# Performance work log

Measured on AMD Instinct MI355X. Metric: run time of the kernel, lower is better.

Reference implementation:

```python
import jax, jax.numpy as jnp
import numpy as np

S, H, I, E, TOP_K = 8192, 2048, 2048, 8, 2


def setup_inputs() -> dict:
    key = jax.random.key(0)
    k0, k1, k2, k3 = jax.random.split(key, 4)
    scale = 1.0 / np.sqrt(H)
    return {
        "hidden_states": jax.random.normal(k0, (S, H), dtype=jnp.float32),
        "w_gate": jax.random.normal(k1, (E, H), dtype=jnp.float32) * scale,
        "w1": jax.random.normal(k2, (E, 2 * I, H), dtype=jnp.float32) * scale,
        "w2": jax.random.normal(k3, (E, H, I), dtype=jnp.float32) * (1.0 / np.sqrt(I)),
        "top_k": TOP_K,
    }


def reference(hidden_states, w_gate, w1, w2, top_k):
    # Router: logits -> float32 softmax -> top-k -> renormalize
    router_logits = hidden_states @ w_gate.T                      # [S, E]
    probs = jax.nn.softmax(router_logits.astype(jnp.float32), axis=-1)
    top_p, top_i = jax.lax.top_k(probs, top_k)                    # [S, k]
    top_p = top_p / jnp.sum(top_p, axis=-1, keepdims=True)

    n_tok, n_exp = probs.shape
    # Dense combine weights [S, E]; zero for non-selected experts.
    combine = jnp.zeros((n_tok, n_exp), dtype=probs.dtype)
    combine = combine.at[jnp.arange(n_tok)[:, None], top_i].add(top_p)

    inter = w2.shape[2]
    out = jnp.zeros_like(hidden_states)
    # Loop over the small fixed expert set; masked-combine gives exact
    # fused_moe semantics (scatter-combine of weighted expert outputs).
    for e in range(n_exp):
        gu = hidden_states @ w1[e].T                              # [S, 2I]
        gate, up = gu[:, :inter], gu[:, inter:]
        h = jax.nn.silu(gate) * up                                # SiluAndMul
        out = out + combine[:, e:e + 1].astype(hidden_states.dtype) * (h @ w2[e].T)
    return out, router_logits
```

## Files before the change

### kernel.cpp

```cpp
#include <hip/hip_runtime.h>
#include <hip/hip_bf16.h>
#include <stdint.h>

#define S_TOK 8192
#define H_DIM 2048
#define I_DIM 2048
#define E_NUM 8

typedef __attribute__((ext_vector_type(4))) float f32x4;
typedef __attribute__((ext_vector_type(8))) short bf16x8;

#define MFMA16(a, b, c) __builtin_amdgcn_mfma_f32_16x16x32_bf16((a), (b), (c), 0, 0, 0)

__device__ __forceinline__ unsigned short f2bf(float f) {
    unsigned int u = __float_as_uint(f);
    unsigned int r = (u + 0x7FFFu + ((u >> 16) & 1u)) >> 16;
    return (unsigned short)r;
}
__device__ __forceinline__ float bf2f(unsigned short u) {
    return __uint_as_float((unsigned int)u << 16);
}

__device__ __forceinline__ void async_copy16(void* lds, const void* g) {
    __builtin_amdgcn_global_load_lds(
        (const __attribute__((address_space(1))) void*)(uintptr_t)g,
        (__attribute__((address_space(3))) void*)(uintptr_t)lds,
        16, 0, 0);
}

__device__ __forceinline__ int xcd_swizzle(int bid, int nwg) {
    int cpx = nwg >> 3;
    return (bid & 7) * cpx + (bid >> 3);
}

__global__ void cvt_kernel(const float* __restrict__ src, unsigned short* __restrict__ dst, long n) {
    long i0 = ((long)blockIdx.x * blockDim.x + threadIdx.x) * 4;
    long stride = (long)gridDim.x * blockDim.x * 4;
    for (long i = i0; i < n; i += stride) {
        float4 v = *(const float4*)(src + i);
        ushort4 o;
        o.x = f2bf(v.x); o.y = f2bf(v.y); o.z = f2bf(v.z); o.w = f2bf(v.w);
        *(ushort4*)(dst + i) = o;
    }
}

__global__ void router_kernel(const float* __restrict__ hs, const float* __restrict__ wg,
                              float* __restrict__ logits, int* __restrict__ cnt,
                              int* __restrict__ tok_of, float* __restrict__ wgt_of,
                              unsigned int* __restrict__ slot_of,
                              unsigned short* __restrict__ hsb) {
    int t = blockIdx.x;
    int tid = threadIdx.x;
    const float* hrow = hs + (size_t)t * H_DIM;
    float4 h0 = *(const float4*)(hrow + tid * 8);
    float4 h1 = *(const float4*)(hrow + tid * 8 + 4);
    ushort4 oA, oB;
    oA.x = f2bf(h0.x); oA.y = f2bf(h0.y); oA.z = f2bf(h0.z); oA.w = f2bf(h0.w);
    oB.x = f2bf(h1.x); oB.y = f2bf(h1.y); oB.z = f2bf(h1.z); oB.w = f2bf(h1.w);
    *(ushort4*)(hsb + (size_t)t * H_DIM + tid * 8) = oA;
    *(ushort4*)(hsb + (size_t)t * H_DIM + tid * 8 + 4) = oB;

    float p[E_NUM];
#pragma unroll
    for (int e = 0; e < E_NUM; ++e) {
        const float* w = wg + (size_t)e * H_DIM + tid * 8;
        float4 w0 = *(const float4*)(w);
        float4 w1v = *(const float4*)(w + 4);
        p[e] = h0.x * w0.x + h0.y * w0.y + h0.z * w0.z + h0.w * w0.w +
               h1.x * w1v.x + h1.y * w1v.y + h1.z * w1v.z + h1.w * w1v.w;
    }
#pragma unroll
    for (int e = 0; e < E_NUM; ++e)
#pragma unroll
        for (int d = 32; d > 0; d >>= 1) p[e] += __shfl_xor(p[e], d, 64);

    __shared__ float red[4][E_NUM];
    int wave = tid >> 6, lane = tid & 63;
    if (lane == 0) {
#pragma unroll
        for (int e = 0; e < E_NUM; ++e) red[wave][e] = p[e];
    }
    __syncthreads();
    if (tid == 0) {
        float l[E_NUM];
#pragma unroll
        for (int e = 0; e < E_NUM; ++e) l[e] = red[0][e] + red[1][e] + red[2][e] + red[3][e];
#pragma unroll
        for (int e = 0; e < E_NUM; ++e) logits[(size_t)t * E_NUM + e] = l[e];
        int i1 = 0;
#pragma unroll
        for (int e = 1; e < E_NUM; ++e) if (l[e] > l[i1]) i1 = e;
        int i2 = (i1 == 0) ? 1 : 0;
#pragma unroll
        for (int e = 0; e < E_NUM; ++e) if (e != i1 && l[e] > l[i2]) i2 = e;
        float b = __expf(l[i2] - l[i1]);
        float wA = 1.0f / (1.0f + b);
        float wB = 1.0f - wA;
        int s1 = atomicAdd(&cnt[i1], 1);
        tok_of[i1 * S_TOK + s1] = t; wgt_of[i1 * S_TOK + s1] = wA;
        int s2 = atomicAdd(&cnt[i2], 1);
        tok_of[i2 * S_TOK + s2] = t; wgt_of[i2 * S_TOK + s2] = wB;
        slot_of[2 * t]     = ((unsigned)i1 << 20) | (unsigned)s1;
        slot_of[2 * t + 1] = ((unsigned)i2 << 20) | (unsigned)s2;
    }
}

__global__ void offsets_kernel(const int* __restrict__ cnt, int* __restrict__ off) {
    if (threadIdx.x == 0) {
        int s = 0;
        for (int e = 0; e < E_NUM; ++e) { off[e] = s; s += cnt[e]; }
    }
}

__global__ void combine_kernel(const unsigned short* __restrict__ pbuf,
                               const unsigned int* __restrict__ slot_of,
                               const int* __restrict__ off, float* __restrict__ out) {
    int t = blockIdx.x, tid = threadIdx.x;
    unsigned int a = slot_of[2 * t], b = slot_of[2 * t + 1];
    size_t ra = (size_t)(off[a >> 20] + (int)(a & 0xFFFFFu));
    size_t rb = (size_t)(off[b >> 20] + (int)(b & 0xFFFFFu));
    const unsigned short* pa = pbuf + ra * H_DIM + tid * 8;
    const unsigned short* pb = pbuf + rb * H_DIM + tid * 8;
    ushort4 a0 = *(const ushort4*)pa, a1 = *(const ushort4*)(pa + 4);
    ushort4 b0 = *(const ushort4*)pb, b1 = *(const ushort4*)(pb + 4);
    float4 r0, r1;
    r0.x = bf2f(a0.x) + bf2f(b0.x); r0.y = bf2f(a0.y) + bf2f(b0.y);
    r0.z = bf2f(a0.z) + bf2f(b0.z); r0.w = bf2f(a0.w) + bf2f(b0.w);
    r1.x = bf2f(a1.x) + bf2f(b1.x); r1.y = bf2f(a1.y) + bf2f(b1.y);
    r1.z = bf2f(a1.z) + bf2f(b1.z); r1.w = bf2f(a1.w) + bf2f(b1.w);
    float* op = out + (size_t)t * H_DIM + tid * 8;
    *(float4*)op = r0;
    *(float4*)(op + 4) = r1;
}

template<int IS_G1>
__global__ __launch_bounds__(512, 2) void moe_gemm_kernel(
    const unsigned short* __restrict__ A_src, const unsigned short* __restrict__ W,
    const int* __restrict__ cnt, const int* __restrict__ off,
    const int* __restrict__ tok_of, const float* __restrict__ wgt_of,
    unsigned short* __restrict__ dst,
    const float* __restrict__ cvt_src, unsigned short* __restrict__ cvt_dst,
    long cvt_n, int gemm_grid, int cvt_blks) {
    if ((int)blockIdx.x >= gemm_grid) {
        long i0 = ((long)((int)blockIdx.x - gemm_grid) * blockDim.x + threadIdx.x) * 4;
        long stride = (long)cvt_blks * blockDim.x * 4;
        for (long i = i0; i < cvt_n; i += stride) {
            float4 v = *(const float4*)(cvt_src + i);
            ushort4 o;
            o.x = f2bf(v.x); o.y = f2bf(v.y); o.z = f2bf(v.z); o.w = f2bf(v.w);
            *(ushort4*)(cvt_dst + i) = o;
        }
        return;
    }
    const int NT = IS_G1 ? 16 : 8;
    int bx = xcd_swizzle(blockIdx.x, gemm_grid);
    int nt = bx / (E_NUM * 32);
    int rr = bx % (E_NUM * 32);
    int e = rr / 32;
    int mt = rr % 32;
    (void)NT;
    int C = cnt[e];
    if (mt * 256 >= C) return;
    int O = off[e];

    __shared__ __align__(16) char ldsA[2][32768];
    __shared__ __align__(16) char ldsB[2][32768];

    int tid = threadIdx.x;
    int wave = tid >> 6, lane = tid & 63;
    int wr = wave >> 2, wc = wave & 3;

    const char* aptr[4];
#pragma unroll
    for (int q = 0; q < 4; ++q) {
        int row = q * 64 + wave * 8 + (lane >> 3);
        int cu = (lane & 7) ^ (row & 7);
        int grow = mt * 256 + row; if (grow > C - 1) grow = C - 1;
        size_t arow = IS_G1 ? (size_t)tok_of[e * S_TOK + grow] : (size_t)(O + grow);
        aptr[q] = (const char*)(A_src + arow * 2048 + cu * 8);
    }
    const char* bptr[4];
#pragma unroll
    for (int j = 0; j < 4; ++j) {
        int lrow = j * 64 + wave * 8 + (lane >> 3);
        int cu = (lane & 7) ^ (lrow & 7);
        int np = lrow >> 7, wcg = (lrow >> 5) & 3, rem = lrow & 31;
        int tbrow = wcg * 64 + np * 32 + rem;
        size_t brow;
        if (IS_G1) {
            int jj = tbrow & 63, wq = tbrow >> 6;
            if (jj < 32) brow = (size_t)(nt * 128 + wq * 32 + jj);
            else         brow = (size_t)I_DIM + nt * 128 + wq * 32 + (jj - 32);
            brow += (size_t)e * (2 * I_DIM);
        } else {
            brow = (size_t)e * H_DIM + nt * 256 + tbrow;
        }
        bptr[j] = (const char*)(W + brow * 2048 + cu * 8);
    }

    int aoff[8][2], boff[4][2];
#pragma unroll
    for (int m = 0; m < 8; ++m)
#pragma unroll
        for (int ks = 0; ks < 2; ++ks) {
            int row = wr * 128 + m * 16 + (lane & 15);
            int cu = ks * 4 + (lane >> 4);
            aoff[m][ks] = row * 128 + ((cu ^ (row & 7)) * 16);
        }
#pragma unroll
    for (int n = 0; n < 4; ++n)
#pragma unroll
        for (int ks = 0; ks < 2; ++ks) {
            int lrow = (n >> 1) * 128 + wc * 32 + (n & 1) * 16 + (lane & 15);
            int cu = ks * 4 + (lane >> 4);
            boff[n][ks] = lrow * 128 + ((cu ^ (lrow & 7)) * 16);
        }

    f32x4 acc[8][4];
#pragma unroll
    for (int m = 0; m < 8; ++m)
#pragma unroll
        for (int n = 0; n < 4; ++n)
#pragma unroll
            for (int q = 0; q < 4; ++q) acc[m][n][q] = 0.0f;

    auto gA = [&](int q, int T, int buf) {
        async_copy16(ldsA[buf] + q * 8192 + wave * 1024, aptr[q] + T * 128);
    };
    auto gB = [&](int j, int T, int buf) {
        async_copy16(ldsB[buf] + j * 8192 + wave * 1024, bptr[j] + T * 128);
    };

    gA(0, 0, 0); gA(2, 0, 0); gA(1, 0, 0); gA(3, 0, 0);
    gB(0, 0, 0); gB(1, 0, 0);
    gA(0, 1, 1); gA(2, 1, 1); gA(1, 1, 1); gA(3, 1, 1);
    gB(2, 0, 0); gB(3, 0, 0);
    asm volatile("s_waitcnt vmcnt(6)" ::: "memory");
    __builtin_amdgcn_s_barrier();

    bf16x8 ar[8][2], br[2][2];
    int cur = 0;
#pragma unroll 2
    for (int T = 0; T < 32; ++T) {
        int nxt = cur ^ 1;
        int TA = (T + 2 < 32) ? T + 2 : 31;
        int TB = (T + 1 < 32) ? T + 1 : 31;
#pragma unroll
        for (int n = 0; n < 2; ++n)
#pragma unroll
            for (int ks = 0; ks < 2; ++ks)
                br[n][ks] = *(const bf16x8*)(ldsB[cur] + boff[n][ks]);
#pragma unroll
        for (int m = 0; m < 4; ++m)
#pragma unroll
            for (int ks = 0; ks < 2; ++ks)
                ar[m][ks] = *(const bf16x8*)(ldsA[cur] + aoff[m][ks]);
        gB(0, TB, nxt); gB(1, TB, nxt);
        __builtin_amdgcn_s_setprio(1);
#pragma unroll
        for (int m = 0; m < 4; ++m)
#pragma unroll
            for (int n = 0; n < 2; ++n) {
                acc[m][n] = MFMA16(ar[m][0], br[n][0], acc[m][n]);
                acc[m][n] = MFMA16(ar[m][1], br[n][1], acc[m][n]);
            }
        __builtin_amdgcn_s_setprio(0);
        __builtin_amdgcn_s_barrier();
#pragma unroll
        for (int m = 4; m < 8; ++m)
#pragma unroll
            for (int ks = 0; ks < 2; ++ks)
                ar[m][ks] = *(const bf16x8*)(ldsA[cur] + aoff[m][ks]);
        gA(0, TA, cur); gA(2, TA, cur);
        __builtin_amdgcn_s_setprio(1);
#pragma unroll
        for (int m = 4; m < 8; ++m)
#pragma unroll
            for (int n = 0; n < 2; ++n) {
                acc[m][n] = MFMA16(ar[m][0], br[n][0], acc[m][n]);
                acc[m][n] = MFMA16(ar[m][1], br[n][1], acc[m][n]);
            }
        __builtin_amdgcn_s_setprio(0);
        asm volatile("s_waitcnt vmcnt(4)" ::: "memory");
        __builtin_amdgcn_s_barrier();
#pragma unroll
        for (int n = 0; n < 2; ++n)
#pragma unroll
            for (int ks = 0; ks < 2; ++ks)
                br[n][ks] = *(const bf16x8*)(ldsB[cur] + boff[n + 2][ks]);
        gA(1, TA, cur); gA(3, TA, cur);
        __builtin_amdgcn_s_setprio(1);
#pragma unroll
        for (int m = 0; m < 4; ++m)
#pragma unroll
            for (int n = 0; n < 2; ++n) {
                acc[m][n + 2] = MFMA16(ar[m][0], br[n][0], acc[m][n + 2]);
                acc[m][n + 2] = MFMA16(ar[m][1], br[n][1], acc[m][n + 2]);
            }
        __builtin_amdgcn_s_setprio(0);
        __builtin_amdgcn_s_barrier();
        gB(2, TB, nxt); gB(3, TB, nxt);
        __builtin_amdgcn_s_setprio(1);
#pragma unroll
        for (int m = 4; m < 8; ++m)
#pragma unroll
            for (int n = 0; n < 2; ++n) {
                acc[m][n + 2] = MFMA16(ar[m][0], br[n][0], acc[m][n + 2]);
                acc[m][n + 2] = MFMA16(ar[m][1], br[n][1], acc[m][n + 2]);
            }
        __builtin_amdgcn_s_setprio(0);
        asm volatile("s_waitcnt vmcnt(6)" ::: "memory");
        __builtin_amdgcn_s_barrier();
        cur = nxt;
    }

    if (IS_G1) {
#pragma unroll
        for (int m = 0; m < 8; ++m)
#pragma unroll
            for (int q = 0; q < 4; ++q) {
                int row = mt * 256 + wr * 128 + m * 16 + (lane >> 4) * 4 + q;
                if (row < C) {
                    float wgt = wgt_of[e * S_TOK + row];
                    unsigned short* hp = dst + (size_t)(O + row) * I_DIM +
                                         nt * 128 + wc * 32 + (lane & 15);
#pragma unroll
                    for (int n = 0; n < 2; ++n) {
                        float g = acc[m][n][q];
                        float u = acc[m][n + 2][q];
                        float hv = (g / (1.0f + __expf(-g))) * u * wgt;
                        hp[n * 16] = f2bf(hv);
                    }
                }
            }
    } else {
#pragma unroll
        for (int m = 0; m < 8; ++m)
#pragma unroll
            for (int q = 0; q < 4; ++q) {
                int row = mt * 256 + wr * 128 + m * 16 + (lane >> 4) * 4 + q;
                if (row < C) {
                    unsigned short* pp = dst + (size_t)(O + row) * H_DIM +
                                         nt * 256 + wc * 64 + (lane & 15);
#pragma unroll
                    for (int n = 0; n < 4; ++n)
                        pp[n * 16] = f2bf(acc[m][n][q]);
                }
            }
    }
}

extern "C" void kernel_launch(void* const* d_in, const int* in_sizes, int n_in,
                              void* d_out, int out_size, void* d_ws, size_t ws_size,
                              hipStream_t stream) {
    const float* hs = (const float*)d_in[0];
    const float* wg = (const float*)d_in[1];
    const float* w1 = (const float*)d_in[2];
    const float* w2 = (const float*)d_in[3];

    float* out = (float*)d_out;
    float* logits = out + (size_t)S_TOK * H_DIM;

    char* ws = (char*)d_ws;
    int* cnt = (int*)ws;
    int* off = (int*)(ws + 256);
    int* tok_of = (int*)(ws + 512);
    float* wgt_of = (float*)(ws + 512 + (size_t)E_NUM * S_TOK * 4);
    unsigned int* slot_of = (unsigned int*)(ws + 512 + (size_t)E_NUM * S_TOK * 8);
    size_t o = 512 + (size_t)E_NUM * S_TOK * 8 + (size_t)S_TOK * 8;
    o = (o + 4095) & ~(size_t)4095;
    unsigned short* hsb = (unsigned short*)(ws + o);  o += (size_t)S_TOK * H_DIM * 2;
    unsigned short* wxb = (unsigned short*)(ws + o);  o += (size_t)E_NUM * 2 * I_DIM * H_DIM * 2;
    unsigned short* hbuf = (unsigned short*)(ws + o); o += (size_t)S_TOK * 2 * I_DIM * 2;
    size_t o_w2 = o;
    size_t need_fused = o_w2 + (size_t)E_NUM * H_DIM * I_DIM * 2;
    bool fused = (ws_size >= need_fused);

    const long W1_N = (long)E_NUM * 2 * I_DIM * H_DIM;
    const long W2_N = (long)E_NUM * H_DIM * I_DIM;
    const int G1_GRID = E_NUM * 32 * 16;
    const int G2_GRID = E_NUM * 32 * 8;
    const int CVT_BLKS = 1024;

    hipMemsetAsync(cnt, 0, 64, stream);
    router_kernel<<<S_TOK, 256, 0, stream>>>(hs, wg, logits, cnt, tok_of, wgt_of, slot_of, hsb);
    offsets_kernel<<<1, 64, 0, stream>>>(cnt, off);
    cvt_kernel<<<4096, 256, 0, stream>>>(w1, wxb, W1_N);

    if (fused) {
        unsigned short* w2b = (unsigned short*)(ws + o_w2);
        unsigned short* pbuf = wxb;
        moe_gemm_kernel<1><<<G1_GRID + CVT_BLKS, 512, 0, stream>>>(
            hsb, wxb, cnt, off, tok_of, wgt_of, hbuf, w2, w2b, W2_N, G1_GRID, CVT_BLKS);
        moe_gemm_kernel<0><<<G2_GRID, 512, 0, stream>>>(
            hbuf, w2b, cnt, off, tok_of, wgt_of, pbuf, nullptr, nullptr, 0, G2_GRID, 0);
        combine_kernel<<<S_TOK, 256, 0, stream>>>(pbuf, slot_of, off, out);
    } else {
        unsigned short* w2b = wxb;
        unsigned short* pbuf = wxb + (size_t)E_NUM * H_DIM * I_DIM;
        moe_gemm_kernel<1><<<G1_GRID, 512, 0, stream>>>(
            hsb, wxb, cnt, off, tok_of, wgt_of, hbuf, nullptr, nullptr, 0, G1_GRID, 0);
        cvt_kernel<<<4096, 256, 0, stream>>>(w2, w2b, W2_N);
        moe_gemm_kernel<0><<<G2_GRID, 512, 0, stream>>>(
            hbuf, w2b, cnt, off, tok_of, wgt_of, pbuf, nullptr, nullptr, 0, G2_GRID, 0);
        combine_kernel<<<S_TOK, 256, 0, stream>>>(pbuf, slot_of, off, out);
    }
}
```

Baseline: 753.7 us.

## Split GEMM1 into halves and overlap W1 second-half conversion with first half

The w1 fp32->bf16 conversion is split into two halves along the N-tile dimension. Only the half needed by the first GEMM1 launch (tiles 0-7) is converted up front, and the second half is converted by extra blocks that run alongside the first GEMM1 half. The w2 conversion moves to ride along with the second GEMM1 half. The conversion loops also now handle 8 elements per thread with 16-byte stores. This hides part of the weight conversion behind matmul work, at the cost of an extra launch and a more complex index mapping.

```diff
diff --git a/kernel.cpp b/kernel.cpp
--- a/kernel.cpp
+++ b/kernel.cpp
@@ -9,6 +9,7 @@
 
 typedef __attribute__((ext_vector_type(4))) float f32x4;
 typedef __attribute__((ext_vector_type(8))) short bf16x8;
+typedef __attribute__((ext_vector_type(8))) unsigned short u16x8;
 
 #define MFMA16(a, b, c) __builtin_amdgcn_mfma_f32_16x16x32_bf16((a), (b), (c), 0, 0, 0)
 
@@ -19,6 +20,15 @@
 }
 __device__ __forceinline__ float bf2f(unsigned short u) {
     return __uint_as_float((unsigned int)u << 16);
+}
+
+__device__ __forceinline__ void cvt8(const float* __restrict__ s, unsigned short* __restrict__ d) {
+    float4 v0 = *(const float4*)s;
+    float4 v1 = *(const float4*)(s + 4);
+    u16x8 o;
+    o[0] = f2bf(v0.x); o[1] = f2bf(v0.y); o[2] = f2bf(v0.z); o[3] = f2bf(v0.w);
+    o[4] = f2bf(v1.x); o[5] = f2bf(v1.y); o[6] = f2bf(v1.z); o[7] = f2bf(v1.w);
+    *(u16x8*)d = o;
 }
 
 __device__ __forceinline__ void async_copy16(void* lds, const void* g) {
@@ -34,14 +44,31 @@
 }
 
 __global__ void cvt_kernel(const float* __restrict__ src, unsigned short* __restrict__ dst, long n) {
-    long i0 = ((long)blockIdx.x * blockDim.x + threadIdx.x) * 4;
-    long stride = (long)gridDim.x * blockDim.x * 4;
-    for (long i = i0; i < n; i += stride) {
-        float4 v = *(const float4*)(src + i);
-        ushort4 o;
-        o.x = f2bf(v.x); o.y = f2bf(v.y); o.z = f2bf(v.z); o.w = f2bf(v.w);
-        *(ushort4*)(dst + i) = o;
-    }
+    long i0 = ((long)blockIdx.x * blockDim.x + threadIdx.x) * 8;
+    long stride = (long)gridDim.x * blockDim.x * 8;
+    for (long i = i0; i < n; i += stride) cvt8(src + i, dst + i);
+}
+
+template<int HALF>
+__device__ __forceinline__ void cvt_w1_half_body(const float* __restrict__ src,
+                                                 unsigned short* __restrict__ dst,
+                                                 long i0, long stride) {
+    const long CH = 1L << 21;
+    const long TOT = (long)E_NUM * 2 * CH;
+    for (long j = i0; j < TOT; j += stride) {
+        long e = j >> 22;
+        long piece = (j >> 21) & 1;
+        long off = j & (CH - 1);
+        long g = (e << 23) + ((piece * 2 + HALF) << 21) + off;
+        cvt8(src + g, dst + g);
+    }
+}
+
+template<int HALF>
+__global__ void cvt_w1_half_kernel(const float* __restrict__ src, unsigned short* __restrict__ dst) {
+    long i0 = ((long)blockIdx.x * blockDim.x + threadIdx.x) * 8;
+    long stride = (long)gridDim.x * blockDim.x * 8;
+    cvt_w1_half_body<HALF>(src, dst, i0, stride);
 }
 
 __global__ void router_kernel(const float* __restrict__ hs, const float* __restrict__ wg,
@@ -54,11 +81,10 @@
     const float* hrow = hs + (size_t)t * H_DIM;
     float4 h0 = *(const float4*)(hrow + tid * 8);
     float4 h1 = *(const float4*)(hrow + tid * 8 + 4);
-    ushort4 oA, oB;
-    oA.x = f2bf(h0.x); oA.y = f2bf(h0.y); oA.z = f2bf(h0.z); oA.w = f2bf(h0.w);
-    oB.x = f2bf(h1.x); oB.y = f2bf(h1.y); oB.z = f2bf(h1.z); oB.w = f2bf(h1.w);
-    *(ushort4*)(hsb + (size_t)t * H_DIM + tid * 8) = oA;
-    *(ushort4*)(hsb + (size_t)t * H_DIM + tid * 8 + 4) = oB;
+    u16x8 o;
+    o[0] = f2bf(h0.x); o[1] = f2bf(h0.y); o[2] = f2bf(h0.z); o[3] = f2bf(h0.w);
+    o[4] = f2bf(h1.x); o[5] = f2bf(h1.y); o[6] = f2bf(h1.z); o[7] = f2bf(h1.w);
+    *(u16x8*)(hsb + (size_t)t * H_DIM + tid * 8) = o;
 
     float p[E_NUM];
 #pragma unroll
@@ -140,25 +166,22 @@
     const int* __restrict__ tok_of, const float* __restrict__ wgt_of,
     unsigned short* __restrict__ dst,
     const float* __restrict__ cvt_src, unsigned short* __restrict__ cvt_dst,
-    long cvt_n, int gemm_grid, int cvt_blks) {
+    long cvt_n, int gemm_grid, int cvt_blks, int nt_base, int cvt_mode) {
     if ((int)blockIdx.x >= gemm_grid) {
-        long i0 = ((long)((int)blockIdx.x - gemm_grid) * blockDim.x + threadIdx.x) * 4;
-        long stride = (long)cvt_blks * blockDim.x * 4;
-        for (long i = i0; i < cvt_n; i += stride) {
-            float4 v = *(const float4*)(cvt_src + i);
-            ushort4 o;
-            o.x = f2bf(v.x); o.y = f2bf(v.y); o.z = f2bf(v.z); o.w = f2bf(v.w);
-            *(ushort4*)(cvt_dst + i) = o;
+        long i0 = ((long)((int)blockIdx.x - gemm_grid) * blockDim.x + threadIdx.x) * 8;
+        long stride = (long)cvt_blks * blockDim.x * 8;
+        if (cvt_mode == 2) {
+            cvt_w1_half_body<1>(cvt_src, cvt_dst, i0, stride);
+        } else {
+            for (long i = i0; i < cvt_n; i += stride) cvt8(cvt_src + i, cvt_dst + i);
         }
         return;
     }
-    const int NT = IS_G1 ? 16 : 8;
     int bx = xcd_swizzle(blockIdx.x, gemm_grid);
-    int nt = bx / (E_NUM * 32);
+    int nt = nt_base + bx / (E_NUM * 32);
     int rr = bx % (E_NUM * 32);
     int e = rr / 32;
     int mt = rr % 32;
-    (void)NT;
     int C = cnt[e];
     if (mt * 256 >= C) return;
     int O = off[e];
@@ -378,31 +401,39 @@
 
     const long W1_N = (long)E_NUM * 2 * I_DIM * H_DIM;
     const long W2_N = (long)E_NUM * H_DIM * I_DIM;
-    const int G1_GRID = E_NUM * 32 * 16;
+    const int G1H_GRID = E_NUM * 32 * 8;
     const int G2_GRID = E_NUM * 32 * 8;
     const int CVT_BLKS = 1024;
 
     hipMemsetAsync(cnt, 0, 64, stream);
     router_kernel<<<S_TOK, 256, 0, stream>>>(hs, wg, logits, cnt, tok_of, wgt_of, slot_of, hsb);
     offsets_kernel<<<1, 64, 0, stream>>>(cnt, off);
-    cvt_kernel<<<4096, 256, 0, stream>>>(w1, wxb, W1_N);
 
     if (fused) {
         unsigned short* w2b = (unsigned short*)(ws + o_w2);
         unsigned short* pbuf = wxb;
-        moe_gemm_kernel<1><<<G1_GRID + CVT_BLKS, 512, 0, stream>>>(
-            hsb, wxb, cnt, off, tok_of, wgt_of, hbuf, w2, w2b, W2_N, G1_GRID, CVT_BLKS);
+        cvt_w1_half_kernel<0><<<4096, 256, 0, stream>>>(w1, wxb);
+        moe_gemm_kernel<1><<<G1H_GRID + CVT_BLKS, 512, 0, stream>>>(
+            hsb, wxb, cnt, off, tok_of, wgt_of, hbuf,
+            w1, wxb, 0, G1H_GRID, CVT_BLKS, 0, 2);
+        moe_gemm_kernel<1><<<G1H_GRID + CVT_BLKS, 512, 0, stream>>>(
+            hsb, wxb, cnt, off, tok_of, wgt_of, hbuf,
+            w2, w2b, W2_N, G1H_GRID, CVT_BLKS, 8, 1);
         moe_gemm_kernel<0><<<G2_GRID, 512, 0, stream>>>(
-            hbuf, w2b, cnt, off, tok_of, wgt_of, pbuf, nullptr, nullptr, 0, G2_GRID, 0);
+            hbuf, w2b, cnt, off, tok_of, wgt_of, pbuf,
+            nullptr, nullptr, 0, G2_GRID, 0, 0, 0);
         combine_kernel<<<S_TOK, 256, 0, stream>>>(pbuf, slot_of, off, out);
     } else {
         unsigned short* w2b = wxb;
         unsigned short* pbuf = wxb + (size_t)E_NUM * H_DIM * I_DIM;
-        moe_gemm_kernel<1><<<G1_GRID, 512, 0, stream>>>(
-            hsb, wxb, cnt, off, tok_of, wgt_of, hbuf, nullptr, nullptr, 0, G1_GRID, 0);
+        cvt_kernel<<<4096, 256, 0, stream>>>(w1, wxb, W1_N);
+        moe_gemm_kernel<1><<<E_NUM * 32 * 16, 512, 0, stream>>>(
+            hsb, wxb, cnt, off, tok_of, wgt_of, hbuf,
+            nullptr, nullptr, 0, E_NUM * 32 * 16, 0, 0, 0);
         cvt_kernel<<<4096, 256, 0, stream>>>(w2, w2b, W2_N);
         moe_gemm_kernel<0><<<G2_GRID, 512, 0, stream>>>(
-            hbuf, w2b, cnt, off, tok_of, wgt_of, pbuf, nullptr, nullptr, 0, G2_GRID, 0);
+            hbuf, w2b, cnt, off, tok_of, wgt_of, pbuf,
+            nullptr, nullptr, 0, G2_GRID, 0, 0, 0);
         combine_kernel<<<S_TOK, 256, 0, stream>>>(pbuf, slot_of, off, out);
     }
 }
```

Result: faster. 738.7 us (-2.0%).
